# Performance work log

Hardware: AMD Instinct MI355X
Metric: run time of the kernel (lower is better)

## Reference

```python
import jax, jax.numpy as jnp
import numpy as np

B, N, H, F = 4, 512, 4096, 11008   # batch, seq, hidden, intermediate
L, R, RANK = 1, 16, 16             # layers stored, num adapters, lora rank
SCALE = 0.5                        # lora_scale


def setup_inputs() -> dict:
    key = jax.random.key(0)
    ks = jax.random.split(key, 12)
    nrm = lambda k, shape, fan: (jax.random.normal(k, shape, jnp.float32) * (fan ** -0.5))
    inp = {
        "x": jax.random.normal(ks[0], (B, N, H), jnp.float32),
        "W_gate": nrm(ks[1], (F, H), H),
        "W_up": nrm(ks[2], (F, H), H),
        "W_down": nrm(ks[3], (H, F), F),
        # LoRA tables: [num_layers, num_adapters, rank, in] and [num_layers, num_adapters, out, rank]
        "A_gate": nrm(ks[4], (L, R, RANK, H), H),
        "B_gate": nrm(ks[5], (L, R, F, RANK), RANK),
        "A_up": nrm(ks[6], (L, R, RANK, H), H),
        "B_up": nrm(ks[7], (L, R, F, RANK), RANK),
        "A_down": nrm(ks[8], (L, R, RANK, F), F),
        "B_down": nrm(ks[9], (L, R, H, RANK), RANK),
        "lora_indices": jax.random.randint(ks[10], (B,), 0, R),
        "layer_idx": 0,
    }
    return inp


def reference(x, W_gate, W_up, W_down, A_gate, B_gate, A_up, B_up,
              A_down, B_down, lora_indices, layer_idx):
    def lora_add(base, inp, A, B):
        # gather per-sequence adapter slices, then rank-r batched matmuls
        Ab = A[layer_idx][lora_indices]  # [B, r, in]
        Bb = B[layer_idx][lora_indices]  # [B, out, r]
        t = jnp.einsum('bri,bni->bnr', Ab, inp)        # down-project to rank
        return base + jnp.einsum('bor,bnr->bno', Bb, t) * SCALE

    gate = lora_add(jnp.einsum('bnh,fh->bnf', x, W_gate), x, A_gate, B_gate)
    up = lora_add(jnp.einsum('bnh,fh->bnf', x, W_up), x, A_up, B_up)
    act = jax.nn.silu(gate) * up                        # SwiGLU
    down = lora_add(jnp.einsum('bnf,hf->bnh', act, W_down), act, A_down, B_down)
    return down
```

## Files before the change

### kernel.cpp

```cpp
#include <hip/hip_runtime.h>
#include <hip/hip_bf16.h>

typedef __bf16 bf16x8 __attribute__((ext_vector_type(8)));
typedef float  f32x4  __attribute__((ext_vector_type(4)));
typedef unsigned short u16;

#define GLDS16(gsrc, ldst)                                                        \
  __builtin_amdgcn_global_load_lds(                                               \
      (const __attribute__((address_space(1))) unsigned int*)(gsrc),              \
      (__attribute__((address_space(3))) unsigned int*)(ldst), 16, 0, 0)

#define BAR() __builtin_amdgcn_s_barrier()
#define WAIT_LGKM0() asm volatile("s_waitcnt lgkmcnt(0)" ::: "memory")
#define WAIT_VM4() asm volatile("s_waitcnt vmcnt(4)" ::: "memory")

__device__ __forceinline__ u16 f2b(float f) {
  unsigned int u = __builtin_bit_cast(unsigned int, f);
  u = (u + 0x7fffu + ((u >> 16) & 1u)) >> 16;
  return (u16)u;
}
__device__ __forceinline__ float b2f(u16 b) {
  unsigned int u = ((unsigned int)b) << 16;
  return __builtin_bit_cast(float, u);
}

__global__ __launch_bounds__(256) void cvt_kernel(const float4* __restrict__ in,
                                                  ushort4* __restrict__ out, int n4) {
  int i = blockIdx.x * blockDim.x + threadIdx.x;
  int stride = gridDim.x * blockDim.x;
  for (; i < n4; i += stride) {
    float4 v = in[i];
    ushort4 o;
    o.x = f2b(v.x); o.y = f2b(v.y); o.z = f2b(v.z); o.w = f2b(v.w);
    out[i] = o;
  }
}

__global__ __launch_bounds__(256) void lora_t2(const u16* __restrict__ Xb, int K,
                                               const float* __restrict__ A1,
                                               const float* __restrict__ A2,
                                               const int* __restrict__ lidx,
                                               const int* __restrict__ layer,
                                               u16* __restrict__ t1,
                                               u16* __restrict__ t2) {
  __shared__ float red1[4][64][4];
  __shared__ float red2[4][64][4];
  const int lane = threadIdx.x & 63, wid = threadIdx.x >> 6;
  const int m0 = blockIdx.x * 16;
  const int li = lidx[m0 >> 9];
  const size_t abase = ((size_t)layer[0] * 16 + li) * 16 * (size_t)K;
  const int r = lane & 15, kg = lane >> 4;
  const int Kq = K >> 2, kb = wid * Kq;
  f32x4 acc1 = {0.f, 0.f, 0.f, 0.f}, acc2 = {0.f, 0.f, 0.f, 0.f};
  for (int k0 = kb; k0 < kb + Kq; k0 += 32) {
    bf16x8 a = *(const bf16x8*)&Xb[(size_t)(m0 + r) * K + k0 + kg * 8];
    const float* ap = A1 + abase + (size_t)r * K + k0 + kg * 8;
    float4 f0 = *(const float4*)ap;
    float4 f1 = *(const float4*)(ap + 4);
    bf16x8 b;
    b[0] = (__bf16)f0.x; b[1] = (__bf16)f0.y; b[2] = (__bf16)f0.z; b[3] = (__bf16)f0.w;
    b[4] = (__bf16)f1.x; b[5] = (__bf16)f1.y; b[6] = (__bf16)f1.z; b[7] = (__bf16)f1.w;
    acc1 = __builtin_amdgcn_mfma_f32_16x16x32_bf16(a, b, acc1, 0, 0, 0);
    if (A2) {
      const float* ap2 = A2 + abase + (size_t)r * K + k0 + kg * 8;
      float4 g0 = *(const float4*)ap2;
      float4 g1 = *(const float4*)(ap2 + 4);
      bf16x8 b2;
      b2[0] = (__bf16)g0.x; b2[1] = (__bf16)g0.y; b2[2] = (__bf16)g0.z; b2[3] = (__bf16)g0.w;
      b2[4] = (__bf16)g1.x; b2[5] = (__bf16)g1.y; b2[6] = (__bf16)g1.z; b2[7] = (__bf16)g1.w;
      acc2 = __builtin_amdgcn_mfma_f32_16x16x32_bf16(a, b2, acc2, 0, 0, 0);
    }
  }
#pragma unroll
  for (int j = 0; j < 4; ++j) {
    red1[wid][lane][j] = acc1[j];
    if (A2) red2[wid][lane][j] = acc2[j];
  }
  __syncthreads();
  if (wid == 0) {
#pragma unroll
    for (int j = 0; j < 4; ++j) {
      int m = m0 + kg * 4 + j;
      float v1 = red1[0][lane][j] + red1[1][lane][j] + red1[2][lane][j] + red1[3][lane][j];
      t1[(size_t)m * 16 + r] = f2b(0.5f * v1);
      if (A2) {
        float v2 = red2[0][lane][j] + red2[1][lane][j] + red2[2][lane][j] + red2[3][lane][j];
        t2[(size_t)m * 16 + r] = f2b(0.5f * v2);
      }
    }
  }
}

#define RD_A(dst, buf, mh) do {                                                \
    _Pragma("unroll")                                                          \
    for (int mf_ = 0; mf_ < 4; ++mf_)                                          \
      _Pragma("unroll")                                                        \
      for (int ks_ = 0; ks_ < 2; ++ks_) {                                      \
        int row_ = wm * 128 + (mh) * 64 + mf_ * 16 + lr;                       \
        int sl_ = (ks_ * 4 + kg) ^ rx;                                         \
        dst[mf_][ks_] = *(const bf16x8*)&sA[(buf) * 16384 + row_ * 64 + sl_ * 8]; \
      }                                                                        \
  } while (0)

#define RD_B(dst, buf, nh) do {                                                \
    _Pragma("unroll")                                                          \
    for (int nf_ = 0; nf_ < 2; ++nf_)                                          \
      _Pragma("unroll")                                                        \
      for (int ks_ = 0; ks_ < 2; ++ks_) {                                      \
        int row_ = wn * 64 + (nh) * 32 + nf_ * 16 + lr;                        \
        int sl_ = (ks_ * 4 + kg) ^ rx;                                         \
        dst[nf_][ks_] = *(const bf16x8*)&sB[(buf) * 16384 + row_ * 64 + sl_ * 8]; \
      }                                                                        \
  } while (0)

#define MMA_Q(AF, BF, mb, nb) do {                                             \
    __builtin_amdgcn_s_setprio(1);                                             \
    _Pragma("unroll")                                                          \
    for (int mf_ = 0; mf_ < 4; ++mf_)                                          \
      _Pragma("unroll")                                                        \
      for (int nf_ = 0; nf_ < 2; ++nf_)                                        \
        _Pragma("unroll")                                                      \
        for (int ks_ = 0; ks_ < 2; ++ks_)                                      \
          acc[(mb) + mf_][(nb) + nf_] = __builtin_amdgcn_mfma_f32_16x16x32_bf16( \
              AF[mf_][ks_], BF[nf_][ks_], acc[(mb) + mf_][(nb) + nf_], 0, 0, 0); \
    __builtin_amdgcn_s_setprio(0);                                             \
  } while (0)

#define STAGE(buf, half, kt) do {                                              \
    int r0_ = ((half) & 1) * 128;                                              \
    const u16* gs_ = ((half) < 2)                                              \
        ? (Xb + (size_t)(m0 + r0_) * 4096 + (size_t)(kt) * 64)                 \
        : (W + (size_t)(n0 + r0_) * 4096 + (size_t)(kt) * 64);                 \
    u16* ld_ = (((half) < 2) ? sA : sB) + (buf) * 16384 + r0_ * 64;            \
    _Pragma("unroll")                                                          \
    for (int i_ = 0; i_ < 2; ++i_) {                                           \
      int ub_ = (wid << 6) + i_ * 512;                                         \
      int un_ = ub_ + lane;                                                    \
      int ur_ = un_ >> 3, us_ = (un_ & 7) ^ (ur_ & 7);                         \
      GLDS16(gs_ + (size_t)ur_ * 4096 + us_ * 8, ld_ + ub_ * 8);               \
    }                                                                          \
  } while (0)

__global__ __launch_bounds__(512, 2) void gemm_gup8(
    const u16* __restrict__ Xb, const u16* __restrict__ Wg, const u16* __restrict__ Wu,
    const u16* __restrict__ tg, const u16* __restrict__ tu,
    const float* __restrict__ Bg, const float* __restrict__ Bu,
    const int* __restrict__ lidx, const int* __restrict__ layer,
    u16* __restrict__ gout, u16* __restrict__ uout,
    const float4* __restrict__ Wdf, ushort4* __restrict__ wdb3) {
  constexpr int F = 11008;
  const int b = blockIdx.x;
  if (b >= 704) {
    int i = (b - 704) * 512 + threadIdx.x;
    for (; i < 11272192; i += 256 * 512) {
      float4 v = Wdf[i];
      ushort4 o;
      o.x = f2b(v.x); o.y = f2b(v.y); o.z = f2b(v.z); o.w = f2b(v.w);
      wdb3[i] = o;
    }
    return;
  }
  const int xcd = b & 7, j = b >> 3;
  const int ny = xcd + 8 * (j >> 3);
  const int mx = j & 7;
  if (ny >= 86) return;
  extern __shared__ u16 smem[];
  u16* sA = smem;
  u16* sB = smem + 32768;
  const int tid = threadIdx.x, lane = tid & 63, wid = tid >> 6;
  const int lr = lane & 15, kg = lane >> 4, rx = lr & 7;
  const int wm = wid >> 2, wn = wid & 3;
  const bool isUp = ny >= 43;
  const int m0 = mx * 256;
  const int n0 = (isUp ? ny - 43 : ny) * 256;
  const u16* W = isUp ? Wu : Wg;
  const u16* tb = isUp ? tu : tg;
  const float* Bw = isUp ? Bu : Bg;
  u16* ob = isUp ? uout : gout;

  f32x4 acc[8][4] = {};
  bf16x8 a0[4][2], a1[4][2], b0[2][2], b1[2][2];

  STAGE(0, 0, 0); STAGE(0, 1, 0); STAGE(0, 2, 0); STAGE(0, 3, 0);
  STAGE(1, 2, 1); STAGE(1, 3, 1);
  WAIT_VM4(); BAR();

#pragma unroll 1
  for (int u = 0; u < 32; ++u) {
    const int ktA = (2 * u + 1) & 63;
    const int kt0 = (2 * u + 2) & 63;
    const int kt1 = (2 * u + 3) & 63;
    RD_A(a0, 0, 0); RD_B(b0, 0, 0);
    STAGE(1, 0, ktA);
    BAR(); WAIT_LGKM0();
    MMA_Q(a0, b0, 0, 0);
    BAR();
    RD_B(b1, 0, 1);
    STAGE(1, 1, ktA);
    BAR(); WAIT_LGKM0();
    MMA_Q(a0, b1, 0, 2);
    BAR();
    RD_A(a1, 0, 1);
    STAGE(0, 2, kt0);
    BAR(); WAIT_LGKM0();
    MMA_Q(a1, b1, 4, 2);
    BAR();
    STAGE(0, 3, kt0);
    BAR();
    MMA_Q(a1, b0, 4, 0);
    WAIT_VM4();
    BAR();
    RD_A(a0, 1, 0); RD_B(b0, 1, 0);
    STAGE(0, 0, kt0);
    BAR(); WAIT_LGKM0();
    MMA_Q(a0, b0, 0, 0);
    BAR();
    RD_B(b1, 1, 1);
    STAGE(0, 1, kt0);
    BAR(); WAIT_LGKM0();
    MMA_Q(a0, b1, 0, 2);
    BAR();
    RD_A(a1, 1, 1);
    STAGE(1, 2, kt1);
    BAR(); WAIT_LGKM0();
    MMA_Q(a1, b1, 4, 2);
    BAR();
    STAGE(1, 3, kt1);
    BAR();
    MMA_Q(a1, b0, 4, 0);
    WAIT_VM4();
    BAR();
  }

  const int li = lidx[m0 >> 9];
  const size_t bbase = ((size_t)layer[0] * 16 + li) * (size_t)F * 16;
  bf16x8 la[8], lb[4];
  const bf16x8 zz = {};
#pragma unroll
  for (int mf = 0; mf < 8; ++mf) {
    int row = m0 + wm * 128 + mf * 16 + lr;
    la[mf] = (kg < 2) ? *(const bf16x8*)&tb[(size_t)row * 16 + kg * 8] : zz;
  }
#pragma unroll
  for (int nf = 0; nf < 4; ++nf) {
    int col = n0 + wn * 64 + nf * 16 + lr;
    if (kg < 2) {
      const float* bp = Bw + bbase + (size_t)col * 16 + kg * 8;
      float4 f0 = *(const float4*)bp;
      float4 f1 = *(const float4*)(bp + 4);
      bf16x8 v;
      v[0] = (__bf16)f0.x; v[1] = (__bf16)f0.y; v[2] = (__bf16)f0.z; v[3] = (__bf16)f0.w;
      v[4] = (__bf16)f1.x; v[5] = (__bf16)f1.y; v[6] = (__bf16)f1.z; v[7] = (__bf16)f1.w;
      lb[nf] = v;
    } else lb[nf] = zz;
  }
#pragma unroll
  for (int mf = 0; mf < 8; ++mf)
#pragma unroll
    for (int nf = 0; nf < 4; ++nf)
      acc[mf][nf] = __builtin_amdgcn_mfma_f32_16x16x32_bf16(la[mf], lb[nf], acc[mf][nf], 0, 0, 0);

#pragma unroll
  for (int mf = 0; mf < 8; ++mf)
#pragma unroll
    for (int nf = 0; nf < 4; ++nf)
#pragma unroll
      for (int j2 = 0; j2 < 4; ++j2) {
        int row = m0 + wm * 128 + mf * 16 + kg * 4 + j2;
        int col = n0 + wn * 64 + nf * 16 + lr;
        ob[(size_t)row * F + col] = f2b(acc[mf][nf][j2]);
      }
}

#define STAGE_D(buf, half, kt) do {                                           \
    int r0_ = ((half) & 1) * 128;                                             \
    const u16* gs_ = ((half) < 2)                                             \
        ? (Ab + (size_t)(m0 + r0_) * 11008 + (size_t)(kt) * 64)               \
        : (Wd + (size_t)(n0 + r0_) * 11008 + (size_t)(kt) * 64);              \
    u16* ld_ = (((half) < 2) ? sA : sB) + (buf) * 16384 + r0_ * 64;           \
    _Pragma("unroll")                                                         \
    for (int i_ = 0; i_ < 2; ++i_) {                                          \
      int ub_ = (wid << 6) + i_ * 512;                                        \
      int un_ = ub_ + lane;                                                   \
      int ur_ = un_ >> 3, us_ = (un_ & 7) ^ (ur_ & 7);                        \
      GLDS16(gs_ + (size_t)ur_ * 11008 + us_ * 8, ld_ + ub_ * 8);             \
    }                                                                         \
  } while (0)

#define KT(t) (kbase + ((t) >= 86 ? (t) - 86 : (t)))

__global__ __launch_bounds__(512, 2) void gemm_down8(
    const u16* __restrict__ Ab, const u16* __restrict__ Wd,
    const u16* __restrict__ td, const float* __restrict__ Bd,
    const int* __restrict__ lidx, const int* __restrict__ layer,
    float* __restrict__ P0, float* __restrict__ P1) {
  constexpr int H = 4096;
  extern __shared__ u16 smem[];
  u16* sA = smem;
  u16* sB = smem + 32768;
  const int tid = threadIdx.x, lane = tid & 63, wid = tid >> 6;
  const int lr = lane & 15, kg = lane >> 4, rx = lr & 7;
  const int wm = wid >> 2, wn = wid & 3;
  const int m0 = blockIdx.x * 256, n0 = blockIdx.y * 256;
  const int kbase = blockIdx.z * 86;
  float* P = blockIdx.z ? P1 : P0;

  f32x4 acc[8][4] = {};
  bf16x8 a0[4][2], a1[4][2], b0[2][2], b1[2][2];

  STAGE_D(0, 0, KT(0)); STAGE_D(0, 1, KT(0)); STAGE_D(0, 2, KT(0)); STAGE_D(0, 3, KT(0));
  STAGE_D(1, 2, KT(1)); STAGE_D(1, 3, KT(1));
  WAIT_VM4(); BAR();

#pragma unroll 1
  for (int u = 0; u < 43; ++u) {
    const int ktA = KT(2 * u + 1);
    const int kt0 = KT(2 * u + 2);
    const int kt1 = KT(2 * u + 3);
    RD_A(a0, 0, 0); RD_B(b0, 0, 0);
    STAGE_D(1, 0, ktA);
    BAR(); WAIT_LGKM0();
    MMA_Q(a0, b0, 0, 0);
    BAR();
    RD_B(b1, 0, 1);
    STAGE_D(1, 1, ktA);
    BAR(); WAIT_LGKM0();
    MMA_Q(a0, b1, 0, 2);
    BAR();
    RD_A(a1, 0, 1);
    STAGE_D(0, 2, kt0);
    BAR(); WAIT_LGKM0();
    MMA_Q(a1, b1, 4, 2);
    BAR();
    STAGE_D(0, 3, kt0);
    BAR();
    MMA_Q(a1, b0, 4, 0);
    WAIT_VM4();
    BAR();
    RD_A(a0, 1, 0); RD_B(b0, 1, 0);
    STAGE_D(0, 0, kt0);
    BAR(); WAIT_LGKM0();
    MMA_Q(a0, b0, 0, 0);
    BAR();
    RD_B(b1, 1, 1);
    STAGE_D(0, 1, kt0);
    BAR(); WAIT_LGKM0();
    MMA_Q(a0, b1, 0, 2);
    BAR();
    RD_A(a1, 1, 1);
    STAGE_D(1, 2, kt1);
    BAR(); WAIT_LGKM0();
    MMA_Q(a1, b1, 4, 2);
    BAR();
    STAGE_D(1, 3, kt1);
    BAR();
    MMA_Q(a1, b0, 4, 0);
    WAIT_VM4();
    BAR();
  }

  if (blockIdx.z == 0) {
    const int li = lidx[m0 >> 9];
    const size_t bbase = ((size_t)layer[0] * 16 + li) * (size_t)H * 16;
    bf16x8 la[8], lb[4];
    const bf16x8 zz = {};
#pragma unroll
    for (int mf = 0; mf < 8; ++mf) {
      int row = m0 + wm * 128 + mf * 16 + lr;
      la[mf] = (kg < 2) ? *(const bf16x8*)&td[(size_t)row * 16 + kg * 8] : zz;
    }
#pragma unroll
    for (int nf = 0; nf < 4; ++nf) {
      int col = n0 + wn * 64 + nf * 16 + lr;
      if (kg < 2) {
        const float* bp = Bd + bbase + (size_t)col * 16 + kg * 8;
        float4 f0 = *(const float4*)bp;
        float4 f1 = *(const float4*)(bp + 4);
        bf16x8 v;
        v[0] = (__bf16)f0.x; v[1] = (__bf16)f0.y; v[2] = (__bf16)f0.z; v[3] = (__bf16)f0.w;
        v[4] = (__bf16)f1.x; v[5] = (__bf16)f1.y; v[6] = (__bf16)f1.z; v[7] = (__bf16)f1.w;
        lb[nf] = v;
      } else lb[nf] = zz;
    }
#pragma unroll
    for (int mf = 0; mf < 8; ++mf)
#pragma unroll
      for (int nf = 0; nf < 4; ++nf)
        acc[mf][nf] = __builtin_amdgcn_mfma_f32_16x16x32_bf16(la[mf], lb[nf], acc[mf][nf], 0, 0, 0);
  }

#pragma unroll
  for (int mf = 0; mf < 8; ++mf)
#pragma unroll
    for (int nf = 0; nf < 4; ++nf)
#pragma unroll
      for (int j = 0; j < 4; ++j) {
        int row = m0 + wm * 128 + mf * 16 + kg * 4 + j;
        int col = n0 + wn * 64 + nf * 16 + lr;
        P[(size_t)row * H + col] = acc[mf][nf][j];
      }
}

__global__ __launch_bounds__(256) void combine_down(
    const float4* __restrict__ P0, const float4* __restrict__ P1,
    float4* __restrict__ out) {
  int gid = blockIdx.x * 256 + threadIdx.x;
  float4 p0 = P0[gid], p1 = P1[gid];
  out[gid] = make_float4(p0.x + p1.x, p0.y + p1.y, p0.z + p1.z, p0.w + p1.w);
}

__global__ __launch_bounds__(256) void swiglu_kernel(uint4* __restrict__ g,
                                                     const uint4* __restrict__ u, int n) {
  int i = blockIdx.x * 256 + threadIdx.x, st = gridDim.x * 256;
  for (; i < n; i += st) {
    uint4 gv = g[i], uv = u[i], ov;
    unsigned* gw = (unsigned*)&gv;
    unsigned* uw = (unsigned*)&uv;
    unsigned* ow = (unsigned*)&ov;
#pragma unroll
    for (int q = 0; q < 4; ++q) {
      float g0 = __builtin_bit_cast(float, gw[q] << 16);
      float g1 = __builtin_bit_cast(float, gw[q] & 0xffff0000u);
      float u0 = __builtin_bit_cast(float, uw[q] << 16);
      float u1 = __builtin_bit_cast(float, uw[q] & 0xffff0000u);
      float a0 = g0 / (1.f + __expf(-g0)) * u0;
      float a1 = g1 / (1.f + __expf(-g1)) * u1;
      ow[q] = (unsigned)f2b(a0) | ((unsigned)f2b(a1) << 16);
    }
    g[i] = ov;
  }
}

extern "C" void kernel_launch(void* const* d_in, const int* in_sizes, int n_in,
                              void* d_out, int out_size, void* d_ws, size_t ws_size,
                              hipStream_t stream) {
  const float* x  = (const float*)d_in[0];
  const float* Wg = (const float*)d_in[1];
  const float* Wu = (const float*)d_in[2];
  const float* Wd = (const float*)d_in[3];
  const float* Ag = (const float*)d_in[4];
  const float* Bg = (const float*)d_in[5];
  const float* Au = (const float*)d_in[6];
  const float* Bu = (const float*)d_in[7];
  const float* Ad = (const float*)d_in[8];
  const float* Bd = (const float*)d_in[9];
  const int* lidx = (const int*)d_in[10];
  const int* lay  = (const int*)d_in[11];
  float* out = (float*)d_out;

  char* ws = (char*)d_ws;
  u16*  xb   = (u16*)(ws + 0);
  u16*  wgb  = (u16*)(ws + 16777216);
  u16*  wub  = (u16*)(ws + 106954752);
  u16*  gbuf = (u16*)(ws + 197132288);
  u16*  ubuf = (u16*)(ws + 242221056);
  u16*  tg   = (u16*)(ws + 287309824);
  u16*  tu   = (u16*)(ws + 287375360);
  u16*  td   = (u16*)(ws + 287440896);
  u16*  wdb3 = (u16*)(ws + 287506432);
  float* P0  = (float*)ubuf;
  float* P1  = (float*)wub;

  hipFuncSetAttribute(reinterpret_cast<const void*>(gemm_gup8),
                      hipFuncAttributeMaxDynamicSharedMemorySize, 131072);
  hipFuncSetAttribute(reinterpret_cast<const void*>(gemm_down8),
                      hipFuncAttributeMaxDynamicSharedMemorySize, 131072);

  cvt_kernel<<<1024, 256, 0, stream>>>((const float4*)x,  (ushort4*)xb,  8388608 / 4);
  cvt_kernel<<<2048, 256, 0, stream>>>((const float4*)Wg, (ushort4*)wgb, 45088768 / 4);
  cvt_kernel<<<2048, 256, 0, stream>>>((const float4*)Wu, (ushort4*)wub, 45088768 / 4);

  lora_t2<<<128, 256, 0, stream>>>(xb, 4096, Ag, Au, lidx, lay, tg, tu);

  gemm_gup8<<<dim3(960), 512, 131072, stream>>>(
      xb, wgb, wub, tg, tu, Bg, Bu, lidx, lay, gbuf, ubuf,
      (const float4*)Wd, (ushort4*)wdb3);

  swiglu_kernel<<<2048, 256, 0, stream>>>((uint4*)gbuf, (const uint4*)ubuf, 2818048);

  lora_t2<<<128, 256, 0, stream>>>(gbuf, 11008, Ad, nullptr, lidx, lay, td, nullptr);

  gemm_down8<<<dim3(8, 16, 2), 512, 131072, stream>>>(gbuf, wdb3, td, Bd, lidx, lay,
                                                      P0, P1);

  combine_down<<<8192, 256, 0, stream>>>((const float4*)P0, (const float4*)P1,
                                         (float4*)out);
}
```

Measured before the change: 768.1 us.

## Fuse gate and up GEMMs with SwiGLU epilogue in one tile

Each block of the gate/up GEMM now computes a 256x128 tile of both the gate and the up projection at once. It shares the X tile in LDS and keeps two accumulator sets, then applies LoRA and SiLU(gate)*up in the epilogue. This removes the separate swiglu kernel and the round trip of writing and re-reading the gate and up buffers. The cost is that each block stages two weight tiles per k-step while the output per block shrinks, so MMA work relative to loads changes.

New measurement: 734.0 us. 1.05x faster.

```diff
diff --git a/kernel.cpp b/kernel.cpp
--- a/kernel.cpp
+++ b/kernel.cpp
@@ -113,6 +113,17 @@
       }                                                                        \
   } while (0)
 
+#define RD_BW(dst, SB, buf) do {                                               \
+    _Pragma("unroll")                                                          \
+    for (int nf_ = 0; nf_ < 2; ++nf_)                                          \
+      _Pragma("unroll")                                                        \
+      for (int ks_ = 0; ks_ < 2; ++ks_) {                                      \
+        int row_ = wn * 32 + nf_ * 16 + lr;                                    \
+        int sl_ = (ks_ * 4 + kg) ^ rx;                                         \
+        dst[nf_][ks_] = *(const bf16x8*)&SB[(buf) * 8192 + row_ * 64 + sl_ * 8]; \
+      }                                                                        \
+  } while (0)
+
 #define MMA_Q(AF, BF, mb, nb) do {                                             \
     __builtin_amdgcn_s_setprio(1);                                             \
     _Pragma("unroll")                                                          \
@@ -126,12 +137,25 @@
     __builtin_amdgcn_s_setprio(0);                                             \
   } while (0)
 
-#define STAGE(buf, half, kt) do {                                              \
-    int r0_ = ((half) & 1) * 128;                                              \
-    const u16* gs_ = ((half) < 2)                                              \
-        ? (Xb + (size_t)(m0 + r0_) * 4096 + (size_t)(kt) * 64)                 \
-        : (W + (size_t)(n0 + r0_) * 4096 + (size_t)(kt) * 64);                 \
-    u16* ld_ = (((half) < 2) ? sA : sB) + (buf) * 16384 + r0_ * 64;            \
+#define MMA_F(AF, BF, ACC, mb) do {                                            \
+    __builtin_amdgcn_s_setprio(1);                                             \
+    _Pragma("unroll")                                                          \
+    for (int mf_ = 0; mf_ < 4; ++mf_)                                          \
+      _Pragma("unroll")                                                        \
+      for (int nf_ = 0; nf_ < 2; ++nf_)                                        \
+        _Pragma("unroll")                                                      \
+        for (int ks_ = 0; ks_ < 2; ++ks_)                                      \
+          ACC[(mb) + mf_][nf_] = __builtin_amdgcn_mfma_f32_16x16x32_bf16(      \
+              AF[mf_][ks_], BF[nf_][ks_], ACC[(mb) + mf_][nf_], 0, 0, 0);      \
+    __builtin_amdgcn_s_setprio(0);                                             \
+  } while (0)
+
+#define STAGE_F(buf, half, kt) do {                                            \
+    const u16* gs_; u16* ld_;                                                  \
+    if ((half) == 0)      { gs_ = Xb + (size_t)m0 * 4096 + (size_t)(kt) * 64;         ld_ = sA  + (buf) * 16384; }        \
+    else if ((half) == 1) { gs_ = Xb + (size_t)(m0 + 128) * 4096 + (size_t)(kt) * 64; ld_ = sA  + (buf) * 16384 + 8192; } \
+    else if ((half) == 2) { gs_ = Wg + (size_t)n0 * 4096 + (size_t)(kt) * 64;         ld_ = sBG + (buf) * 8192; }         \
+    else                  { gs_ = Wu + (size_t)n0 * 4096 + (size_t)(kt) * 64;         ld_ = sBU + (buf) * 8192; }         \
     _Pragma("unroll")                                                          \
     for (int i_ = 0; i_ < 2; ++i_) {                                           \
       int ub_ = (wid << 6) + i_ * 512;                                         \
@@ -141,12 +165,12 @@
     }                                                                          \
   } while (0)
 
-__global__ __launch_bounds__(512, 2) void gemm_gup8(
+__global__ __launch_bounds__(512, 2) void gemm_gup_fused(
     const u16* __restrict__ Xb, const u16* __restrict__ Wg, const u16* __restrict__ Wu,
     const u16* __restrict__ tg, const u16* __restrict__ tu,
     const float* __restrict__ Bg, const float* __restrict__ Bu,
     const int* __restrict__ lidx, const int* __restrict__ layer,
-    u16* __restrict__ gout, u16* __restrict__ uout,
+    u16* __restrict__ act,
     const float4* __restrict__ Wdf, ushort4* __restrict__ wdb3) {
   constexpr int F = 11008;
   const int b = blockIdx.x;
@@ -165,24 +189,20 @@
   const int mx = j & 7;
   if (ny >= 86) return;
   extern __shared__ u16 smem[];
-  u16* sA = smem;
-  u16* sB = smem + 32768;
+  u16* sA  = smem;
+  u16* sBG = smem + 32768;
+  u16* sBU = smem + 49152;
   const int tid = threadIdx.x, lane = tid & 63, wid = tid >> 6;
   const int lr = lane & 15, kg = lane >> 4, rx = lr & 7;
   const int wm = wid >> 2, wn = wid & 3;
-  const bool isUp = ny >= 43;
   const int m0 = mx * 256;
-  const int n0 = (isUp ? ny - 43 : ny) * 256;
-  const u16* W = isUp ? Wu : Wg;
-  const u16* tb = isUp ? tu : tg;
-  const float* Bw = isUp ? Bu : Bg;
-  u16* ob = isUp ? uout : gout;
-
-  f32x4 acc[8][4] = {};
-  bf16x8 a0[4][2], a1[4][2], b0[2][2], b1[2][2];
-
-  STAGE(0, 0, 0); STAGE(0, 1, 0); STAGE(0, 2, 0); STAGE(0, 3, 0);
-  STAGE(1, 2, 1); STAGE(1, 3, 1);
+  const int n0 = ny * 128;
+
+  f32x4 accg[8][2] = {}, accu[8][2] = {};
+  bf16x8 a0[4][2], a1[4][2], bg[2][2], bu[2][2];
+
+  STAGE_F(0, 0, 0); STAGE_F(0, 1, 0); STAGE_F(0, 2, 0); STAGE_F(0, 3, 0);
+  STAGE_F(1, 2, 1); STAGE_F(1, 3, 1);
   WAIT_VM4(); BAR();
 
 #pragma unroll 1
@@ -190,62 +210,62 @@
     const int ktA = (2 * u + 1) & 63;
     const int kt0 = (2 * u + 2) & 63;
     const int kt1 = (2 * u + 3) & 63;
-    RD_A(a0, 0, 0); RD_B(b0, 0, 0);
-    STAGE(1, 0, ktA);
-    BAR(); WAIT_LGKM0();
-    MMA_Q(a0, b0, 0, 0);
-    BAR();
-    RD_B(b1, 0, 1);
-    STAGE(1, 1, ktA);
-    BAR(); WAIT_LGKM0();
-    MMA_Q(a0, b1, 0, 2);
+    RD_A(a0, 0, 0); RD_BW(bg, sBG, 0);
+    STAGE_F(1, 0, ktA);
+    BAR(); WAIT_LGKM0();
+    MMA_F(a0, bg, accg, 0);
+    BAR();
+    RD_BW(bu, sBU, 0);
+    STAGE_F(1, 1, ktA);
+    BAR(); WAIT_LGKM0();
+    MMA_F(a0, bu, accu, 0);
     BAR();
     RD_A(a1, 0, 1);
-    STAGE(0, 2, kt0);
-    BAR(); WAIT_LGKM0();
-    MMA_Q(a1, b1, 4, 2);
-    BAR();
-    STAGE(0, 3, kt0);
-    BAR();
-    MMA_Q(a1, b0, 4, 0);
+    STAGE_F(0, 2, kt0);
+    BAR(); WAIT_LGKM0();
+    MMA_F(a1, bu, accu, 4);
+    BAR();
+    STAGE_F(0, 3, kt0);
+    BAR();
+    MMA_F(a1, bg, accg, 4);
     WAIT_VM4();
     BAR();
-    RD_A(a0, 1, 0); RD_B(b0, 1, 0);
-    STAGE(0, 0, kt0);
-    BAR(); WAIT_LGKM0();
-    MMA_Q(a0, b0, 0, 0);
-    BAR();
-    RD_B(b1, 1, 1);
-    STAGE(0, 1, kt0);
-    BAR(); WAIT_LGKM0();
-    MMA_Q(a0, b1, 0, 2);
+    RD_A(a0, 1, 0); RD_BW(bg, sBG, 1);
+    STAGE_F(0, 0, kt0);
+    BAR(); WAIT_LGKM0();
+    MMA_F(a0, bg, accg, 0);
+    BAR();
+    RD_BW(bu, sBU, 1);
+    STAGE_F(0, 1, kt0);
+    BAR(); WAIT_LGKM0();
+    MMA_F(a0, bu, accu, 0);
     BAR();
     RD_A(a1, 1, 1);
-    STAGE(1, 2, kt1);
-    BAR(); WAIT_LGKM0();
-    MMA_Q(a1, b1, 4, 2);
-    BAR();
-    STAGE(1, 3, kt1);
-    BAR();
-    MMA_Q(a1, b0, 4, 0);
+    STAGE_F(1, 2, kt1);
+    BAR(); WAIT_LGKM0();
+    MMA_F(a1, bu, accu, 4);
+    BAR();
+    STAGE_F(1, 3, kt1);
+    BAR();
+    MMA_F(a1, bg, accg, 4);
     WAIT_VM4();
     BAR();
   }
 
   const int li = lidx[m0 >> 9];
   const size_t bbase = ((size_t)layer[0] * 16 + li) * (size_t)F * 16;
-  bf16x8 la[8], lb[4];
+  bf16x8 la[8], lb[2];
   const bf16x8 zz = {};
 #pragma unroll
   for (int mf = 0; mf < 8; ++mf) {
     int row = m0 + wm * 128 + mf * 16 + lr;
-    la[mf] = (kg < 2) ? *(const bf16x8*)&tb[(size_t)row * 16 + kg * 8] : zz;
-  }
-#pragma unroll
-  for (int nf = 0; nf < 4; ++nf) {
-    int col = n0 + wn * 64 + nf * 16 + lr;
+    la[mf] = (kg < 2) ? *(const bf16x8*)&tg[(size_t)row * 16 + kg * 8] : zz;
+  }
+#pragma unroll
+  for (int nf = 0; nf < 2; ++nf) {
+    int col = n0 + wn * 32 + nf * 16 + lr;
     if (kg < 2) {
-      const float* bp = Bw + bbase + (size_t)col * 16 + kg * 8;
+      const float* bp = Bg + bbase + (size_t)col * 16 + kg * 8;
       float4 f0 = *(const float4*)bp;
       float4 f1 = *(const float4*)(bp + 4);
       bf16x8 v;
@@ -257,18 +277,43 @@
 #pragma unroll
   for (int mf = 0; mf < 8; ++mf)
 #pragma unroll
-    for (int nf = 0; nf < 4; ++nf)
-      acc[mf][nf] = __builtin_amdgcn_mfma_f32_16x16x32_bf16(la[mf], lb[nf], acc[mf][nf], 0, 0, 0);
-
+    for (int nf = 0; nf < 2; ++nf)
+      accg[mf][nf] = __builtin_amdgcn_mfma_f32_16x16x32_bf16(la[mf], lb[nf], accg[mf][nf], 0, 0, 0);
+#pragma unroll
+  for (int mf = 0; mf < 8; ++mf) {
+    int row = m0 + wm * 128 + mf * 16 + lr;
+    la[mf] = (kg < 2) ? *(const bf16x8*)&tu[(size_t)row * 16 + kg * 8] : zz;
+  }
+#pragma unroll
+  for (int nf = 0; nf < 2; ++nf) {
+    int col = n0 + wn * 32 + nf * 16 + lr;
+    if (kg < 2) {
+      const float* bp = Bu + bbase + (size_t)col * 16 + kg * 8;
+      float4 f0 = *(const float4*)bp;
+      float4 f1 = *(const float4*)(bp + 4);
+      bf16x8 v;
+      v[0] = (__bf16)f0.x; v[1] = (__bf16)f0.y; v[2] = (__bf16)f0.z; v[3] = (__bf16)f0.w;
+      v[4] = (__bf16)f1.x; v[5] = (__bf16)f1.y; v[6] = (__bf16)f1.z; v[7] = (__bf16)f1.w;
+      lb[nf] = v;
+    } else lb[nf] = zz;
+  }
 #pragma unroll
   for (int mf = 0; mf < 8; ++mf)
 #pragma unroll
-    for (int nf = 0; nf < 4; ++nf)
+    for (int nf = 0; nf < 2; ++nf)
+      accu[mf][nf] = __builtin_amdgcn_mfma_f32_16x16x32_bf16(la[mf], lb[nf], accu[mf][nf], 0, 0, 0);
+
+#pragma unroll
+  for (int mf = 0; mf < 8; ++mf)
+#pragma unroll
+    for (int nf = 0; nf < 2; ++nf)
 #pragma unroll
       for (int j2 = 0; j2 < 4; ++j2) {
         int row = m0 + wm * 128 + mf * 16 + kg * 4 + j2;
-        int col = n0 + wn * 64 + nf * 16 + lr;
-        ob[(size_t)row * F + col] = f2b(acc[mf][nf][j2]);
+        int col = n0 + wn * 32 + nf * 16 + lr;
+        float g = accg[mf][nf][j2], uu = accu[mf][nf][j2];
+        float s = g / (1.f + __expf(-g));
+        act[(size_t)row * F + col] = f2b(s * uu);
       }
 }
 
@@ -407,28 +452,6 @@
   int gid = blockIdx.x * 256 + threadIdx.x;
   float4 p0 = P0[gid], p1 = P1[gid];
   out[gid] = make_float4(p0.x + p1.x, p0.y + p1.y, p0.z + p1.z, p0.w + p1.w);
-}
-
-__global__ __launch_bounds__(256) void swiglu_kernel(uint4* __restrict__ g,
-                                                     const uint4* __restrict__ u, int n) {
-  int i = blockIdx.x * 256 + threadIdx.x, st = gridDim.x * 256;
-  for (; i < n; i += st) {
-    uint4 gv = g[i], uv = u[i], ov;
-    unsigned* gw = (unsigned*)&gv;
-    unsigned* uw = (unsigned*)&uv;
-    unsigned* ow = (unsigned*)&ov;
-#pragma unroll
-    for (int q = 0; q < 4; ++q) {
-      float g0 = __builtin_bit_cast(float, gw[q] << 16);
-      float g1 = __builtin_bit_cast(float, gw[q] & 0xffff0000u);
-      float u0 = __builtin_bit_cast(float, uw[q] << 16);
-      float u1 = __builtin_bit_cast(float, uw[q] & 0xffff0000u);
-      float a0 = g0 / (1.f + __expf(-g0)) * u0;
-      float a1 = g1 / (1.f + __expf(-g1)) * u1;
-      ow[q] = (unsigned)f2b(a0) | ((unsigned)f2b(a1) << 16);
-    }
-    g[i] = ov;
-  }
 }
 
 extern "C" void kernel_launch(void* const* d_in, const int* in_sizes, int n_in,
@@ -453,15 +476,14 @@
   u16*  wgb  = (u16*)(ws + 16777216);
   u16*  wub  = (u16*)(ws + 106954752);
   u16*  gbuf = (u16*)(ws + 197132288);
-  u16*  ubuf = (u16*)(ws + 242221056);
   u16*  tg   = (u16*)(ws + 287309824);
   u16*  tu   = (u16*)(ws + 287375360);
   u16*  td   = (u16*)(ws + 287440896);
   u16*  wdb3 = (u16*)(ws + 287506432);
-  float* P0  = (float*)ubuf;
+  float* P0  = (float*)(ws + 242221056);
   float* P1  = (float*)wub;
 
-  hipFuncSetAttribute(reinterpret_cast<const void*>(gemm_gup8),
+  hipFuncSetAttribute(reinterpret_cast<const void*>(gemm_gup_fused),
                       hipFuncAttributeMaxDynamicSharedMemorySize, 131072);
   hipFuncSetAttribute(reinterpret_cast<const void*>(gemm_down8),
                       hipFuncAttributeMaxDynamicSharedMemorySize, 131072);
@@ -472,11 +494,9 @@
 
   lora_t2<<<128, 256, 0, stream>>>(xb, 4096, Ag, Au, lidx, lay, tg, tu);
 
-  gemm_gup8<<<dim3(960), 512, 131072, stream>>>(
-      xb, wgb, wub, tg, tu, Bg, Bu, lidx, lay, gbuf, ubuf,
+  gemm_gup_fused<<<dim3(960), 512, 131072, stream>>>(
+      xb, wgb, wub, tg, tu, Bg, Bu, lidx, lay, gbuf,
       (const float4*)Wd, (ushort4*)wdb3);
-
-  swiglu_kernel<<<2048, 256, 0, stream>>>((uint4*)gbuf, (const uint4*)ubuf, 2818048);
 
   lora_t2<<<128, 256, 0, stream>>>(gbuf, 11008, Ad, nullptr, lidx, lay, td, nullptr);
 
```
